# Kernel tuning notes

Hardware: AMD Instinct MI355X
Metric: run time of the kernel (lower is better)

## Reference

```python
import jax, jax.numpy as jnp
import numpy as np

D_MODEL = 1024
NUM_HEADS = 16
HEAD_DIM = D_MODEL // NUM_HEADS
CAUSAL = True


def rope_cos_sin(seq_len, dim):
    inv_freq = 1.0 / (10000.0 ** (jnp.arange(0, dim, 2, dtype=jnp.float32) / dim))
    t = jnp.arange(seq_len, dtype=jnp.float32)
    freqs = jnp.einsum('i,j->ij', t, inv_freq)          # [S, dim/2]
    emb = jnp.concatenate([freqs, freqs], axis=-1)      # [S, dim]
    return jnp.cos(emb), jnp.sin(emb)


def rotate_half(x):
    x1, x2 = jnp.split(x, 2, axis=-1)
    return jnp.concatenate([-x2, x1], axis=-1)


def setup_inputs() -> dict:
    key = jax.random.key(0)
    k1, k2, k3, k4, k5 = jax.random.split(key, 5)
    B, S = 2, 2048
    x = jax.random.normal(k1, (B, S, D_MODEL), dtype=jnp.float32)
    s = 1.0 / np.sqrt(D_MODEL)
    W_qkv = jax.random.normal(k2, (D_MODEL, 3 * D_MODEL), dtype=jnp.float32) * s
    b_qkv = jax.random.normal(k3, (3 * D_MODEL,), dtype=jnp.float32) * 0.01
    W_out = jax.random.normal(k4, (D_MODEL, D_MODEL), dtype=jnp.float32) * s
    b_out = jax.random.normal(k5, (D_MODEL,), dtype=jnp.float32) * 0.01
    return {"x": x, "W_qkv": W_qkv, "b_qkv": b_qkv, "W_out": W_out, "b_out": b_out}


def reference(x, W_qkv, b_qkv, W_out, b_out):
    B, S, _ = x.shape
    qkv = x @ W_qkv + b_qkv                              # [B, S, 3D]
    q, k, v = jnp.split(qkv, 3, axis=-1)
    # [B, H, S, hd]
    q = q.reshape(B, S, NUM_HEADS, HEAD_DIM).transpose(0, 2, 1, 3)
    k = k.reshape(B, S, NUM_HEADS, HEAD_DIM).transpose(0, 2, 1, 3)
    v = v.reshape(B, S, NUM_HEADS, HEAD_DIM).transpose(0, 2, 1, 3)
    cos, sin = rope_cos_sin(S, HEAD_DIM)                 # [S, hd]
    cos = cos[None, None]
    sin = sin[None, None]
    q = q * cos + rotate_half(q) * sin
    k = k * cos + rotate_half(k) * sin
    scores = jnp.einsum('bhqd,bhkd->bhqk', q, k) / np.sqrt(HEAD_DIM)
    if CAUSAL:
        causal_mask = jnp.triu(jnp.ones((S, S), dtype=bool), k=1)
        scores = jnp.where(causal_mask, -jnp.inf, scores)
    attn = jax.nn.softmax(scores, axis=-1)
    out = jnp.einsum('bhqk,bhkd->bhqd', attn, v)         # [B, H, S, hd]
    out = out.transpose(0, 2, 1, 3).reshape(B, S, D_MODEL)
    return out @ W_out + b_out
```

## Files before the change

### kernel.cpp

```cpp
#include <hip/hip_runtime.h>
#include <hip/hip_bf16.h>
#include <math.h>

typedef __bf16 bf16;
typedef __bf16 bf16x8 __attribute__((ext_vector_type(8)));
typedef unsigned short ushort8 __attribute__((ext_vector_type(8)));
typedef float floatx4 __attribute__((ext_vector_type(4)));

#define MFMA_BF16(a, b, c) __builtin_amdgcn_mfma_f32_16x16x32_bf16(a, b, c, 0, 0, 0)

__device__ __forceinline__ bf16x8 cvt8(const float4 a, const float4 b) {
  bf16x8 t;
  t[0] = (bf16)a.x; t[1] = (bf16)a.y; t[2] = (bf16)a.z; t[3] = (bf16)a.w;
  t[4] = (bf16)b.x; t[5] = (bf16)b.y; t[6] = (bf16)b.z; t[7] = (bf16)b.w;
  return t;
}

__device__ __forceinline__ unsigned int pack2(float a, float b) {
  unsigned short lo = __builtin_bit_cast(unsigned short, (bf16)a);
  unsigned short hi = __builtin_bit_cast(unsigned short, (bf16)b);
  return (unsigned int)lo | ((unsigned int)hi << 16);
}

__device__ __forceinline__ void gld16(const bf16* g, bf16* l) {
  __builtin_amdgcn_global_load_lds(
      (const __attribute__((address_space(1))) unsigned int*)g,
      (__attribute__((address_space(3))) unsigned int*)l, 16, 0, 0);
}

__global__ __launch_bounds__(256) void cast_x_kernel(const float* __restrict__ in,
                                                     bf16* __restrict__ out) {
  const int i = blockIdx.x * 256 + threadIdx.x;
  const float4 a = *(const float4*)&in[(size_t)i * 8];
  const float4 b = *(const float4*)&in[(size_t)i * 8 + 4];
  *(bf16x8*)&out[(size_t)i * 8] = cvt8(a, b);
}

__global__ __launch_bounds__(256) void transpose_w_kernel(
    const float* __restrict__ in, bf16* __restrict__ out, int N, int K) {
  __shared__ __align__(16) bf16 T[64][40];
  const int t = threadIdx.x;
  const int k0 = blockIdx.y * 32, n0 = blockIdx.x * 64;
  {
    const int k = t >> 3, n8 = (t & 7) * 8;
    const float* p = &in[(size_t)(k0 + k) * N + n0 + n8];
    const float4 a = *(const float4*)p;
    const float4 b = *(const float4*)(p + 4);
    const float v[8] = {a.x, a.y, a.z, a.w, b.x, b.y, b.z, b.w};
#pragma unroll
    for (int j = 0; j < 8; j++) {
      const int n = n8 + j;
      T[n][k ^ (8 * ((n >> 3) & 3))] = (bf16)v[j];
    }
  }
  __syncthreads();
  {
    const int n = t >> 2, k8 = (t & 3) * 8;
    const int kp = k8 ^ (8 * ((n >> 3) & 3));
    *(bf16x8*)&out[(size_t)(n0 + n) * K + k0 + k8] = *(const bf16x8*)&T[n][kp];
  }
}

template <int TN, int MODE>
__global__ __launch_bounds__(256) void gemm_kernel(
    const bf16* __restrict__ A, const bf16* __restrict__ Bt,
    const float* __restrict__ bias, void* __restrict__ out0,
    bf16* __restrict__ outK, bf16* __restrict__ outV, int M, int N, int K) {
  constexpr int NI = TN / 32;
  constexpr int BI = TN / 32;
  __shared__ __align__(16) bf16 As2[2][128][32];
  __shared__ __align__(16) bf16 Bs2[2][TN][32];

  const int tid = threadIdx.x, lane = tid & 63, w = tid >> 6;
  const int c = lane & 15, quad = lane >> 4;
  const int wm = w >> 1, wn = w & 1;
  const int m0 = blockIdx.y * 128, n0 = blockIdx.x * TN;
  const int srow = lane >> 2, scol = (lane & 3) * 8;

  floatx4 acc[4][NI] = {};

  for (int k0 = 0; k0 < K; k0 += 64) {
    __syncthreads();
#pragma unroll
    for (int i = 0; i < 4; i++) {
      const int seg = w * 4 + i;
      const int kh = seg >> 3, r0 = (seg & 7) * 16;
      gld16(&A[(size_t)(m0 + r0 + srow) * K + k0 + kh * 32 + scol],
            &As2[kh][r0][0]);
    }
#pragma unroll
    for (int i = 0; i < BI; i++) {
      const int seg = w * BI + i;
      const int kh = seg / (TN / 16), r0 = (seg % (TN / 16)) * 16;
      gld16(&Bt[(size_t)(n0 + r0 + srow) * K + k0 + kh * 32 + scol],
            &Bs2[kh][r0][0]);
    }
    __syncthreads();

#pragma unroll
    for (int kh = 0; kh < 2; kh++) {
      bf16x8 af[4], bfr[NI];
#pragma unroll
      for (int mi = 0; mi < 4; mi++)
        af[mi] = *(const bf16x8*)&As2[kh][wm * 64 + mi * 16 + c][quad * 8];
#pragma unroll
      for (int ni = 0; ni < NI; ni++)
        bfr[ni] = *(const bf16x8*)&Bs2[kh][wn * (TN / 2) + ni * 16 + c][quad * 8];
#pragma unroll
      for (int mi = 0; mi < 4; mi++)
#pragma unroll
        for (int ni = 0; ni < NI; ni++)
          acc[mi][ni] = MFMA_BF16(af[mi], bfr[ni], acc[mi][ni]);
    }
  }

#pragma unroll
  for (int mi = 0; mi < 4; mi++) {
#pragma unroll
    for (int ni = 0; ni < NI; ni++) {
#pragma unroll
      for (int r = 0; r < 4; r++) {
        const int row = m0 + wm * 64 + mi * 16 + quad * 4 + r;
        const int col = n0 + wn * (TN / 2) + ni * 16 + c;
        const float v = acc[mi][ni][r] + bias[col];
        if (MODE == 0) {
          ((float*)out0)[(size_t)row * N + col] = v;
        } else {
          const int t = col >> 10;
          const int h = (col & 1023) >> 6;
          const int d = col & 63;
          const int b = row >> 11, s = row & 2047;
          bf16* dst = (t == 0) ? (bf16*)out0 : (t == 1 ? outK : outV);
          dst[(((size_t)b * 16 + h) * 2048 + s) * 64 + d] = (bf16)v;
        }
      }
    }
  }
}

__global__ __launch_bounds__(256) void rope_kernel(bf16* __restrict__ Q,
                                                   bf16* __restrict__ Kt) {
  const int idx = blockIdx.x * 256 + threadIdx.x;
  const int d = idx & 31;
  const int h = (idx >> 5) & 15;
  const int s = (idx >> 9) & 2047;
  const int b = idx >> 20;
  const size_t base = (((size_t)b * 16 + h) * 2048 + s) * 64 + d;

  const float inv = exp2f(-0.41524101186092f * (float)d);
  const float ang = (float)s * inv;
  float sn, cs;
  sincosf(ang, &sn, &cs);

  const float q1 = (float)Q[base], q2 = (float)Q[base + 32];
  const float k1 = (float)Kt[base], k2 = (float)Kt[base + 32];
  Q[base]       = (bf16)((q1 * cs - q2 * sn) * 0.125f);
  Q[base + 32]  = (bf16)((q2 * cs + q1 * sn) * 0.125f);
  Kt[base]      = (bf16)(k1 * cs - k2 * sn);
  Kt[base + 32] = (bf16)(k2 * cs + k1 * sn);
}

struct AttnState {
  floatx4 o[4];
  float l;
};

__device__ __forceinline__ void attn_step(
    const bf16x8 qf[2], const bf16x8 kf[4][2], const bf16x8 vf[4][2],
    bf16 (*PsW)[72], AttnState& st, int qglob, int kbase, bool diag, int c,
    int quad) {
  floatx4 sacc[4] = {};
#pragma unroll
  for (int kg = 0; kg < 4; kg++)
#pragma unroll
    for (int dh = 0; dh < 2; dh++)
      sacc[kg] = MFMA_BF16(kf[kg][dh], qf[dh], sacc[kg]);

#pragma unroll
  for (int kg = 0; kg < 4; kg++) {
    float p[4];
#pragma unroll
    for (int r = 0; r < 4; r++) {
      float e = __expf(sacc[kg][r]);
      if (diag && (kbase + kg * 16 + quad * 4 + r > qglob)) e = 0.0f;
      p[r] = e;
    }
    st.l += (p[0] + p[1]) + (p[2] + p[3]);
    const uint2 u = {pack2(p[0], p[1]), pack2(p[2], p[3])};
    *(uint2*)&PsW[c][kg * 16 + quad * 4] = u;
  }

  bf16x8 pf[2];
#pragma unroll
  for (int ks = 0; ks < 2; ks++)
    pf[ks] = *(const bf16x8*)&PsW[c][ks * 32 + quad * 8];

#pragma unroll
  for (int dg = 0; dg < 4; dg++)
#pragma unroll
    for (int ks = 0; ks < 2; ks++)
      st.o[dg] = MFMA_BF16(vf[dg][ks], pf[ks], st.o[dg]);
}

__global__ __launch_bounds__(256) void attn_kernel(const bf16* __restrict__ Q,
                                                   const bf16* __restrict__ K,
                                                   const bf16* __restrict__ V,
                                                   bf16* __restrict__ Aout) {
  const int S = 2048;
  const int bh = blockIdx.y;
  const int p = blockIdx.x;
  const int tid = threadIdx.x, lane = tid & 63, wave = tid >> 6;
  const int c = lane & 15, quad = lane >> 4;

  __shared__ __align__(16) bf16 Ks2[2][64][32];
  __shared__ __align__(16) bf16 Vt[64][72];
  __shared__ __align__(16) bf16 Ps[4][16][72];

  const bf16* Qb = Q + (size_t)bh * S * 64;
  const bf16* Kb = K + (size_t)bh * S * 64;
  const bf16* Vb = V + (size_t)bh * S * 64;
  const int b = bh >> 4, h = bh & 15;

  const int qA = p, qB = 31 - p;
  const int qgA = qA * 64 + wave * 16 + c;
  const int qgB = qB * 64 + wave * 16 + c;

  bf16x8 qfA[2], qfB[2];
#pragma unroll
  for (int dh = 0; dh < 2; dh++) {
    qfA[dh] = *(const bf16x8*)&Qb[(size_t)qgA * 64 + dh * 32 + quad * 8];
    qfB[dh] = *(const bf16x8*)&Qb[(size_t)qgB * 64 + dh * 32 + quad * 8];
  }

  AttnState stA = {}, stB = {};

  const int vcc = (tid & 7) * 8;
  const int vr2 = ((tid >> 3) + 4 * (tid & 7)) & 31;
  const int ksr = lane >> 2, ksc = (lane & 3) * 8;

  for (int kt = 0; kt <= qB; kt++) {
    __syncthreads();
#pragma unroll
    for (int i = 0; i < 2; i++) {
      const int seg = wave * 2 + i;
      const int dh = seg >> 2, r0 = (seg & 3) * 16;
      gld16(&Kb[(size_t)(kt * 64 + r0 + ksr) * 64 + dh * 32 + ksc],
            &Ks2[dh][r0][0]);
    }
    {
      const bf16* vs = &Vb[(size_t)(kt * 64 + 2 * vr2) * 64 + vcc];
      const ushort8 w0 = __builtin_bit_cast(ushort8, *(const bf16x8*)vs);
      const ushort8 w1 = __builtin_bit_cast(ushort8, *(const bf16x8*)(vs + 64));
#pragma unroll
      for (int j = 0; j < 8; j++)
        *(unsigned int*)&Vt[vcc + j][2 * vr2] =
            (unsigned int)w0[j] | ((unsigned int)w1[j] << 16);
    }
    __syncthreads();

    bf16x8 kf[4][2];
#pragma unroll
    for (int kg = 0; kg < 4; kg++)
#pragma unroll
      for (int dh = 0; dh < 2; dh++)
        kf[kg][dh] = *(const bf16x8*)&Ks2[dh][kg * 16 + c][quad * 8];

    bf16x8 vf[4][2];
#pragma unroll
    for (int dg = 0; dg < 4; dg++)
#pragma unroll
      for (int ks = 0; ks < 2; ks++)
        vf[dg][ks] = *(const bf16x8*)&Vt[dg * 16 + c][ks * 32 + quad * 8];

    attn_step(qfB, kf, vf, Ps[wave], stB, qgB, kt * 64, kt == qB, c, quad);
    if (kt <= qA)
      attn_step(qfA, kf, vf, Ps[wave], stA, qgA, kt * 64, kt == qA, c, quad);
  }

  stA.l += __shfl_xor(stA.l, 16);
  stA.l += __shfl_xor(stA.l, 32);
  stB.l += __shfl_xor(stB.l, 16);
  stB.l += __shfl_xor(stB.l, 32);
  const float ivA = 1.0f / stA.l, ivB = 1.0f / stB.l;

#pragma unroll
  for (int dg = 0; dg < 4; dg++) {
    const uint2 uA = {pack2(stA.o[dg][0] * ivA, stA.o[dg][1] * ivA),
                      pack2(stA.o[dg][2] * ivA, stA.o[dg][3] * ivA)};
    const uint2 uB = {pack2(stB.o[dg][0] * ivB, stB.o[dg][1] * ivB),
                      pack2(stB.o[dg][2] * ivB, stB.o[dg][3] * ivB)};
    *(uint2*)&Aout[((size_t)b * 2048 + qgA) * 1024 + h * 64 + dg * 16 + quad * 4] = uA;
    *(uint2*)&Aout[((size_t)b * 2048 + qgB) * 1024 + h * 64 + dg * 16 + quad * 4] = uB;
  }
}

extern "C" void kernel_launch(void* const* d_in, const int* in_sizes, int n_in,
                              void* d_out, int out_size, void* d_ws,
                              size_t ws_size, hipStream_t stream) {
  const float* x = (const float*)d_in[0];
  const float* W_qkv = (const float*)d_in[1];
  const float* b_qkv = (const float*)d_in[2];
  const float* W_out = (const float*)d_in[3];
  const float* b_out = (const float*)d_in[4];
  float* out = (float*)d_out;

  const int B = 2, S = 2048, NH = 16;
  const size_t qn = (size_t)B * NH * S * 64;

  bf16* xb = (bf16*)d_ws;
  bf16* Wqkvt = xb + qn;
  bf16* Wot = Wqkvt + 3072 * 1024;
  bf16* Qw = Wot + 1024 * 1024;
  bf16* Kw = Qw + qn;
  bf16* Vw = Kw + qn;
  bf16* AO = xb;

  cast_x_kernel<<<dim3(qn / 8 / 256), 256, 0, stream>>>(x, xb);
  transpose_w_kernel<<<dim3(3072 / 64, 1024 / 32), 256, 0, stream>>>(
      W_qkv, Wqkvt, 3072, 1024);
  transpose_w_kernel<<<dim3(1024 / 64, 1024 / 32), 256, 0, stream>>>(
      W_out, Wot, 1024, 1024);

  gemm_kernel<128, 1><<<dim3(3072 / 128, 4096 / 128), 256, 0, stream>>>(
      xb, Wqkvt, b_qkv, Qw, Kw, Vw, 4096, 3072, 1024);
  rope_kernel<<<dim3((B * S * NH * 32) / 256), 256, 0, stream>>>(Qw, Kw);
  attn_kernel<<<dim3(16, B * NH), 256, 0, stream>>>(Qw, Kw, Vw, AO);
  gemm_kernel<64, 0><<<dim3(1024 / 64, 4096 / 128), 256, 0, stream>>>(
      AO, Wot, b_out, out, nullptr, nullptr, 4096, 1024, 1024);
}
```

Baseline: 205.9 us.

## Fuse RoPE into QKV GEMM epilogue and use exp2 with folded log2e scale

Removes the standalone RoPE kernel by applying the rotary embedding in the QKV GEMM epilogue, where each wave's 64-column tile holds a full head so the d and d+32 pairs are in registers. The Q scale now folds log2(e) into 1/sqrt(64), so attention softmax can use the hardware exp2 directly instead of __expf. Also uses the packed bf16 conversion builtin when available. This saves a full read-modify-write pass over Q and K, but adds sincos work to the GEMM epilogue and changes the rounding order (RoPE is applied before the bf16 cast).

```diff
diff --git a/kernel.cpp b/kernel.cpp
--- a/kernel.cpp
+++ b/kernel.cpp
@@ -8,6 +8,15 @@
 typedef float floatx4 __attribute__((ext_vector_type(4)));
 
 #define MFMA_BF16(a, b, c) __builtin_amdgcn_mfma_f32_16x16x32_bf16(a, b, c, 0, 0, 0)
+
+#define Q_SCALE 0.18033688011112042f
+#define NEG_INVFREQ_LOG2 0.41524101186092029f
+
+#if __has_builtin(__builtin_amdgcn_exp2f)
+#define EXP2F(x) __builtin_amdgcn_exp2f(x)
+#else
+#define EXP2F(x) exp2f(x)
+#endif
 
 __device__ __forceinline__ bf16x8 cvt8(const float4 a, const float4 b) {
   bf16x8 t;
@@ -17,9 +26,13 @@
 }
 
 __device__ __forceinline__ unsigned int pack2(float a, float b) {
+#if __has_builtin(__builtin_amdgcn_cvt_pk_bf16_f32)
+  return __builtin_bit_cast(unsigned int, __builtin_amdgcn_cvt_pk_bf16_f32(a, b));
+#else
   unsigned short lo = __builtin_bit_cast(unsigned short, (bf16)a);
   unsigned short hi = __builtin_bit_cast(unsigned short, (bf16)b);
   return (unsigned int)lo | ((unsigned int)hi << 16);
+#endif
 }
 
 __device__ __forceinline__ void gld16(const bf16* g, bf16* l) {
@@ -114,50 +127,60 @@
     }
   }
 
-#pragma unroll
-  for (int mi = 0; mi < 4; mi++) {
-#pragma unroll
-    for (int ni = 0; ni < NI; ni++) {
-#pragma unroll
-      for (int r = 0; r < 4; r++) {
-        const int row = m0 + wm * 64 + mi * 16 + quad * 4 + r;
-        const int col = n0 + wn * (TN / 2) + ni * 16 + c;
-        const float v = acc[mi][ni][r] + bias[col];
-        if (MODE == 0) {
-          ((float*)out0)[(size_t)row * N + col] = v;
-        } else {
-          const int t = col >> 10;
-          const int h = (col & 1023) >> 6;
-          const int d = col & 63;
+  if (MODE == 0) {
+#pragma unroll
+    for (int mi = 0; mi < 4; mi++)
+#pragma unroll
+      for (int ni = 0; ni < NI; ni++)
+#pragma unroll
+        for (int r = 0; r < 4; r++) {
+          const int row = m0 + wm * 64 + mi * 16 + quad * 4 + r;
+          const int col = n0 + wn * (TN / 2) + ni * 16 + c;
+          ((float*)out0)[(size_t)row * N + col] = acc[mi][ni][r] + bias[col];
+        }
+  } else {
+    const int colb = n0 + wn * (TN / 2);
+    const int t = colb >> 10;
+    const int h = (colb & 1023) >> 6;
+    bf16* dst = (t == 0) ? (bf16*)out0 : (t == 1 ? outK : outV);
+    if (t == 2) {
+#pragma unroll
+      for (int mi = 0; mi < 4; mi++)
+#pragma unroll
+        for (int ni = 0; ni < NI; ni++)
+#pragma unroll
+          for (int r = 0; r < 4; r++) {
+            const int row = m0 + wm * 64 + mi * 16 + quad * 4 + r;
+            const int col = colb + ni * 16 + c;
+            const int b = row >> 11, s = row & 2047;
+            dst[(((size_t)b * 16 + h) * 2048 + s) * 64 + (col & 63)] =
+                (bf16)(acc[mi][ni][r] + bias[col]);
+          }
+    } else {
+      const float qs = (t == 0) ? Q_SCALE : 1.0f;
+      const float inv[2] = {exp2f(-NEG_INVFREQ_LOG2 * (float)c),
+                            exp2f(-NEG_INVFREQ_LOG2 * (float)(16 + c))};
+#pragma unroll
+      for (int mi = 0; mi < 4; mi++) {
+#pragma unroll
+        for (int r = 0; r < 4; r++) {
+          const int row = m0 + wm * 64 + mi * 16 + quad * 4 + r;
           const int b = row >> 11, s = row & 2047;
-          bf16* dst = (t == 0) ? (bf16*)out0 : (t == 1 ? outK : outV);
-          dst[(((size_t)b * 16 + h) * 2048 + s) * 64 + d] = (bf16)v;
+          const size_t base = (((size_t)b * 16 + h) * 2048 + s) * 64;
+#pragma unroll
+          for (int ni = 0; ni < 2; ni++) {
+            float sn, cs;
+            sincosf((float)s * inv[ni], &sn, &cs);
+            const float v1 = acc[mi][ni][r] + bias[colb + ni * 16 + c];
+            const float v2 = acc[mi][ni + 2][r] + bias[colb + (ni + 2) * 16 + c];
+            const int d = ni * 16 + c;
+            dst[base + d] = (bf16)((v1 * cs - v2 * sn) * qs);
+            dst[base + d + 32] = (bf16)((v2 * cs + v1 * sn) * qs);
+          }
         }
       }
     }
   }
-}
-
-__global__ __launch_bounds__(256) void rope_kernel(bf16* __restrict__ Q,
-                                                   bf16* __restrict__ Kt) {
-  const int idx = blockIdx.x * 256 + threadIdx.x;
-  const int d = idx & 31;
-  const int h = (idx >> 5) & 15;
-  const int s = (idx >> 9) & 2047;
-  const int b = idx >> 20;
-  const size_t base = (((size_t)b * 16 + h) * 2048 + s) * 64 + d;
-
-  const float inv = exp2f(-0.41524101186092f * (float)d);
-  const float ang = (float)s * inv;
-  float sn, cs;
-  sincosf(ang, &sn, &cs);
-
-  const float q1 = (float)Q[base], q2 = (float)Q[base + 32];
-  const float k1 = (float)Kt[base], k2 = (float)Kt[base + 32];
-  Q[base]       = (bf16)((q1 * cs - q2 * sn) * 0.125f);
-  Q[base + 32]  = (bf16)((q2 * cs + q1 * sn) * 0.125f);
-  Kt[base]      = (bf16)(k1 * cs - k2 * sn);
-  Kt[base + 32] = (bf16)(k2 * cs + k1 * sn);
 }
 
 struct AttnState {
@@ -181,7 +204,7 @@
     float p[4];
 #pragma unroll
     for (int r = 0; r < 4; r++) {
-      float e = __expf(sacc[kg][r]);
+      float e = EXP2F(sacc[kg][r]);
       if (diag && (kbase + kg * 16 + quad * 4 + r > qglob)) e = 0.0f;
       p[r] = e;
     }
@@ -323,7 +346,6 @@
 
   gemm_kernel<128, 1><<<dim3(3072 / 128, 4096 / 128), 256, 0, stream>>>(
       xb, Wqkvt, b_qkv, Qw, Kw, Vw, 4096, 3072, 1024);
-  rope_kernel<<<dim3((B * S * NH * 32) / 256), 256, 0, stream>>>(Qw, Kw);
   attn_kernel<<<dim3(16, B * NH), 256, 0, stream>>>(Qw, Kw, Vw, AO);
   gemm_kernel<64, 0><<<dim3(1024 / 64, 4096 / 128), 256, 0, stream>>>(
       AO, Wot, b_out, out, nullptr, nullptr, 4096, 1024, 1024);
```

After: 203.0 us. No clear change (-1.5%).
